# Performance work log

Measured on AMD Instinct MI355X. Metric: run time of the kernel, lower is better.

The kernel has to match this reference:

```python
import jax, jax.numpy as jnp
import numpy as np

B, D, H, C, V, SAMPLE_NUM = 4096, 1024, 512, 50, 4, 10000


def ds_combin_two(alpha1, alpha2, K):
    """Dempster-Shafer combination of two Dirichlet parameter sets [B, K]."""
    S1 = jnp.sum(alpha1, axis=1, keepdims=True)
    S2 = jnp.sum(alpha2, axis=1, keepdims=True)
    b1 = (alpha1 - 1.0) / S1
    b2 = (alpha2 - 1.0) / S2
    u1 = K / S1  # [B,1]
    u2 = K / S2
    # bb_sum - bb_diag computed without materializing [B,K,K] outer product:
    # sum_ij b1_i b2_j = sum(b1)*sum(b2); diag sum = sum_i b1_i b2_i
    Cconf = jnp.sum(b1, axis=1) * jnp.sum(b2, axis=1) - jnp.sum(b1 * b2, axis=1)  # [B]
    denom = (1.0 - Cconf)[:, None]
    b_a = (b1 * b2 + b1 * u2 + b2 * u1) / denom
    u_a = (u1 * u2) / denom  # [B,1]
    S_a = K / u_a
    e_a = b_a * S_a
    return e_a + 1.0


def setup_inputs() -> dict:
    key = jax.random.key(0)
    ks = jax.random.split(key, 8)
    x = jax.random.normal(ks[0], (V, B, D), dtype=jnp.float32)
    indexes = jax.random.randint(ks[1], (B,), 0, SAMPLE_NUM)
    W1 = jax.random.normal(ks[2], (V, D, H), dtype=jnp.float32) * (1.0 / np.sqrt(D))
    b1 = jax.random.normal(ks[3], (V, H), dtype=jnp.float32) * 0.01
    W2 = jax.random.normal(ks[4], (V, H, C), dtype=jnp.float32) * (1.0 / np.sqrt(H))
    b2 = jax.random.normal(ks[5], (V, C), dtype=jnp.float32) * 0.01
    # original init: identity per (view, sample); add small noise so the
    eye = jnp.eye(C, dtype=jnp.float32)
    matrixes = eye[None, None] + 0.01 * jax.random.normal(ks[6], (V, SAMPLE_NUM, C, C), dtype=jnp.float32)
    return {"x": x, "indexes": indexes, "W1": W1, "b1": b1, "W2": W2, "b2": b2, "matrixes": matrixes}


def reference(x, indexes, W1, b1, W2, b2, matrixes):
    K = W2.shape[-1]
    n_views = x.shape[0]
    # per-view classifier MLP: Linear->ReLU->Linear->Softplus
    h = jax.nn.relu(jnp.einsum("vbd,vdh->vbh", x, W1) + b1[:, None, :])
    evidence = jax.nn.softplus(jnp.einsum("vbh,vhc->vbc", h, W2) + b2[:, None, :])  # [V,B,C]
    # transferByMatrix (training path): per-sample gathered [C,C] matmul
    sel = matrixes[:, indexes]  # [V,B,C,C]
    transferred = jnp.einsum("vbc,vbcd->vbd", evidence, sel)  # [V,B,C]
    t_alpha = transferred + 1.0
    # sequential DS combination over views
    alpha_a = t_alpha[0]
    for v in range(1, n_views):
        alpha_a = ds_combin_two(alpha_a, t_alpha[v], K)
    evidence_a = alpha_a - 1.0  # [B,C]
    return transferred, evidence_a, evidence
```

## Files before the change

kernel.cpp:

```cpp
#include <hip/hip_runtime.h>
#include <hip/hip_bf16.h>
#include <math.h>

typedef unsigned short u16;
typedef __attribute__((ext_vector_type(8))) short bf16x8;
typedef __attribute__((ext_vector_type(4))) float f32x4;

#define DEVI __device__ __forceinline__

constexpr int NV = 4;
constexpr int NB = 4096;
constexpr int ND = 1024;
constexpr int NH = 512;
constexpr int NC = 50;
constexpr int NSAMP = 10000;
constexpr int NCP = 64;

DEVI u16 to_bf16(float f) {
  union { float f; unsigned u; } v; v.f = f;
  unsigned r = v.u + 0x7fffu + ((v.u >> 16) & 1u);
  return (u16)(r >> 16);
}

DEVI u16 cvt_bf16(float f) {
  __hip_bfloat16 h = __float2bfloat16(f);
  return *reinterpret_cast<u16*>(&h);
}

DEVI float wsum(float x) {
#pragma unroll
  for (int m = 32; m > 0; m >>= 1) x += __shfl_xor(x, m, 64);
  return x;
}

#define GLD_LDS16(gsrc, ldst)                                                  \
  __builtin_amdgcn_global_load_lds(                                            \
      (const __attribute__((address_space(1))) void*)(gsrc),                   \
      (__attribute__((address_space(3))) void*)(ldst), 16, 0, 0)

__global__ __launch_bounds__(256) void k_prep(const float* __restrict__ W1,
                                              const float* __restrict__ W2,
                                              u16* __restrict__ W1T,
                                              u16* __restrict__ W2T) {
  __shared__ float tile[32][33];
  const int v = blockIdx.z;
  const int tx = threadIdx.x, ty = threadIdx.y;
  if (blockIdx.y < NH / 32) {
    const int d0 = blockIdx.x * 32;
    const int h0 = blockIdx.y * 32;
    const float* src = W1 + (size_t)v * ND * NH;
    u16* dst = W1T + (size_t)v * NH * ND;
#pragma unroll
    for (int j = 0; j < 32; j += 8)
      tile[ty + j][tx] = src[(size_t)(d0 + ty + j) * NH + h0 + tx];
    __syncthreads();
#pragma unroll
    for (int j = 0; j < 32; j += 8)
      dst[(size_t)(h0 + ty + j) * ND + d0 + tx] = to_bf16(tile[tx][ty + j]);
  } else {
    const int tid = ty * 32 + tx;
#pragma unroll
    for (int i = 0; i < 4; ++i) {
      int e = blockIdx.x * 1024 + i * 256 + tid;
      int h = e % NH;
      int c = e / NH;
      float val = (c < NC) ? W2[((size_t)v * NH + h) * NC + c] : 0.f;
      W2T[(size_t)v * NCP * NH + e] = to_bf16(val);
    }
  }
}

__global__ __launch_bounds__(512) void k_gemm1(const float* __restrict__ Xf,
                                               const u16* __restrict__ W1T,
                                               const float* __restrict__ b1,
                                               u16* __restrict__ Hb) {
  constexpr int BM = 128, BN = 256, BK = 32;
  const int v = blockIdx.z;
  const int m0 = blockIdx.x * BM;
  const int n0 = blockIdx.y * BN;
  __shared__ u16 As[BM][BK];
  __shared__ u16 Bs[BN][BK];
  const float* Ag = Xf + (size_t)v * NB * ND + (size_t)m0 * ND;
  const u16* Bg = W1T + (size_t)v * NH * ND + (size_t)n0 * ND;
  const int tid = threadIdx.x;
  const int lane = tid & 63;
  const int wv = tid >> 6;
  const int wr = wv >> 2, wc = wv & 3;
  const int rA = tid >> 2;
  const int cA = (tid & 3) * 8;

  f32x4 acc[4][4] = {};

  float4 pa0 = *(const float4*)(Ag + (size_t)rA * ND + cA);
  float4 pa1 = *(const float4*)(Ag + (size_t)rA * ND + cA + 4);

  for (int k0 = 0; k0 < ND; k0 += BK) {
    __syncthreads();
    {
      ushort4 u0, u1;
      u0.x = cvt_bf16(pa0.x); u0.y = cvt_bf16(pa0.y);
      u0.z = cvt_bf16(pa0.z); u0.w = cvt_bf16(pa0.w);
      u1.x = cvt_bf16(pa1.x); u1.y = cvt_bf16(pa1.y);
      u1.z = cvt_bf16(pa1.z); u1.w = cvt_bf16(pa1.w);
      *(ushort4*)&As[rA][cA]     = u0;
      *(ushort4*)&As[rA][cA + 4] = u1;
    }
#pragma unroll
    for (int i = 0; i < 2; ++i) {
      int s = tid + i * 512;
      GLD_LDS16(Bg + (size_t)(s >> 2) * ND + k0 + (s & 3) * 8,
                &Bs[s >> 2][(s & 3) * 8]);
    }
    __syncthreads();

    if (k0 + BK < ND) {
      pa0 = *(const float4*)(Ag + (size_t)rA * ND + k0 + BK + cA);
      pa1 = *(const float4*)(Ag + (size_t)rA * ND + k0 + BK + cA + 4);
    }

    const int fr = lane & 15;
    const int kb = (lane >> 4) * 8;
    bf16x8 af[4], bf[4];
#pragma unroll
    for (int mi = 0; mi < 4; ++mi)
      af[mi] = *(const bf16x8*)&As[wr * 64 + mi * 16 + fr][kb];
#pragma unroll
    for (int ni = 0; ni < 4; ++ni)
      bf[ni] = *(const bf16x8*)&Bs[wc * 64 + ni * 16 + fr][kb];
#pragma unroll
    for (int mi = 0; mi < 4; ++mi)
#pragma unroll
      for (int ni = 0; ni < 4; ++ni)
        acc[mi][ni] = __builtin_amdgcn_mfma_f32_16x16x32_bf16(
            af[mi], bf[ni], acc[mi][ni], 0, 0, 0);
  }

  const int frow = (lane >> 4) * 4;
  const int fcol = lane & 15;
#pragma unroll
  for (int mi = 0; mi < 4; ++mi) {
#pragma unroll
    for (int ni = 0; ni < 4; ++ni) {
      const int n = n0 + wc * 64 + ni * 16 + fcol;
      const float bias = b1[v * NH + n];
#pragma unroll
      for (int j = 0; j < 4; ++j) {
        const int m = m0 + wr * 64 + mi * 16 + frow + j;
        float val = fmaxf(acc[mi][ni][j] + bias, 0.f);
        Hb[(size_t)v * NB * NH + (size_t)m * NH + n] = to_bf16(val);
      }
    }
  }
}

__global__ __launch_bounds__(256) void k_gemm2(const u16* __restrict__ Hb,
                                               const u16* __restrict__ W2T,
                                               const float* __restrict__ b2,
                                               float* __restrict__ out_ev) {
  constexpr int BM = 64, BK = 32;
  const int v = blockIdx.z;
  const int m0 = blockIdx.x * BM;
  __shared__ u16 As[BM][BK];
  __shared__ u16 Bs[NCP][BK];
  const u16* Ag = Hb + (size_t)v * NB * NH + (size_t)m0 * NH;
  const u16* Bg = W2T + (size_t)v * NCP * NH;
  const int tid = threadIdx.x;
  const int lane = tid & 63;
  const int wv = tid >> 6;
  const int r = tid >> 2;
  const int c8 = (tid & 3) * 8;

  f32x4 acc[4] = {};

  for (int k0 = 0; k0 < NH; k0 += BK) {
    __syncthreads();
    GLD_LDS16(Ag + (size_t)r * NH + k0 + c8, &As[r][c8]);
    GLD_LDS16(Bg + (size_t)r * NH + k0 + c8, &Bs[r][c8]);
    __syncthreads();

    const int fr = lane & 15;
    const int kb = (lane >> 4) * 8;
    bf16x8 af = *(const bf16x8*)&As[wv * 16 + fr][kb];
#pragma unroll
    for (int ni = 0; ni < 4; ++ni) {
      bf16x8 bf = *(const bf16x8*)&Bs[ni * 16 + fr][kb];
      acc[ni] = __builtin_amdgcn_mfma_f32_16x16x32_bf16(af, bf, acc[ni], 0, 0, 0);
    }
  }

  const int frow = (lane >> 4) * 4;
  const int fcol = lane & 15;
#pragma unroll
  for (int ni = 0; ni < 4; ++ni) {
    const int n = ni * 16 + fcol;
    if (n < NC) {
      const float bias = b2[v * NC + n];
#pragma unroll
      for (int j = 0; j < 4; ++j) {
        const int m = m0 + wv * 16 + frow + j;
        float x = acc[ni][j] + bias;
        float sp = fmaxf(x, 0.f) + log1pf(expf(-fabsf(x)));
        out_ev[(size_t)v * NB * NC + (size_t)m * NC + n] = sp;
      }
    }
  }
}

__global__ __launch_bounds__(256) void k_tc(const float* __restrict__ evf,
                                            const float* __restrict__ mats,
                                            const int* __restrict__ idx,
                                            float* __restrict__ out_tr,
                                            float* __restrict__ out_ea) {
  const int b = blockIdx.x * 4 + (threadIdx.x >> 6);
  const int lane = threadIdx.x & 63;
  if (b >= NB) return;
  const bool act = lane < NC;
  const float Kf = (float)NC;
  const int ix = idx[b];

  float ta[NV];
#pragma unroll
  for (int v = 0; v < NV; ++v) {
    float acc = 0.f;
    if (act) {
      const float* e = evf + ((size_t)v * NB + b) * NC;
      const float* M = mats + ((size_t)v * NSAMP + ix) * NC * NC;
#pragma unroll
      for (int c = 0; c < NC; ++c)
        acc = fmaf(e[c], M[c * NC + lane], acc);
      out_tr[((size_t)v * NB + b) * NC + lane] = acc;
    }
    ta[v] = act ? acc + 1.0f : 0.0f;
  }

  float alpha = ta[0];
#pragma unroll
  for (int v = 1; v < NV; ++v) {
    float a2 = ta[v];
    float S1 = wsum(act ? alpha : 0.f);
    float S2 = wsum(act ? a2 : 0.f);
    float b1v = act ? (alpha - 1.f) / S1 : 0.f;
    float b2v = act ? (a2 - 1.f) / S2 : 0.f;
    float u1 = Kf / S1, u2 = Kf / S2;
    float sb1 = wsum(b1v);
    float sb2 = wsum(b2v);
    float sb12 = wsum(b1v * b2v);
    float Cconf = sb1 * sb2 - sb12;
    float denom = 1.f - Cconf;
    float b_a = (b1v * b2v + b1v * u2 + b2v * u1) / denom;
    float u_a = u1 * u2 / denom;
    float S_a = Kf / u_a;
    alpha = b_a * S_a + 1.f;
  }
  if (act) out_ea[(size_t)b * NC + lane] = alpha - 1.f;
}

extern "C" void kernel_launch(void* const* d_in, const int* in_sizes, int n_in,
                              void* d_out, int out_size, void* d_ws, size_t ws_size,
                              hipStream_t stream) {
  const float *x = nullptr, *W1 = nullptr, *b1 = nullptr, *W2 = nullptr,
              *b2 = nullptr, *mats = nullptr;
  const int* idx = nullptr;
  for (int i = 0; i < n_in; ++i) {
    switch (in_sizes[i]) {
      case 16777216:  x    = (const float*)d_in[i]; break;
      case 4096:      idx  = (const int*)d_in[i];   break;
      case 2097152:   W1   = (const float*)d_in[i]; break;
      case 2048:      b1   = (const float*)d_in[i]; break;
      case 102400:    W2   = (const float*)d_in[i]; break;
      case 200:       b2   = (const float*)d_in[i]; break;
      case 100000000: mats = (const float*)d_in[i]; break;
      default: break;
    }
  }
  if (!x || !idx || !W1 || !b1 || !W2 || !b2 || !mats) return;

  char* ws = (char*)d_ws;
  u16* w1t = (u16*)(ws + 0);
  u16* w2t = (u16*)(ws + 4194304);
  u16* hb  = (u16*)(ws + 4456448);

  float* out_tr = (float*)d_out;
  float* out_ea = out_tr + (size_t)NV * NB * NC;
  float* out_ev = out_ea + (size_t)NB * NC;

  k_prep<<<dim3(32, NH / 32 + 1, NV), dim3(32, 8), 0, stream>>>(W1, W2, w1t, w2t);
  k_gemm1<<<dim3(NB / 128, NH / 256, NV), 512, 0, stream>>>(x, w1t, b1, hb);
  k_gemm2<<<dim3(NB / 64, 1, NV), 256, 0, stream>>>(hb, w2t, b2, out_ev);
  k_tc<<<NB / 4, 256, 0, stream>>>(out_ev, mats, idx, out_tr, out_ea);
}
```

Baseline: 89.41 us.

## Double-buffer LDS tiles in first GEMM with manual waitcnt pipelining

Converts the first GEMM's main loop to a double-buffered LDS pipeline. The next tile of A and B is staged into the alternate buffer while the current one is computed, using explicit s_waitcnt, s_barrier and sched_barrier to control overlap. The aim is to hide global-load and LDS-store latency behind the MFMA work and to drop one barrier per iteration. This doubles LDS use and depends on hand-counted vmcnt/lgkmcnt values, which makes a race possible if the counts are wrong.

```diff
diff --git a/kernel.cpp b/kernel.cpp
--- a/kernel.cpp
+++ b/kernel.cpp
@@ -75,11 +75,12 @@
                                                const float* __restrict__ b1,
                                                u16* __restrict__ Hb) {
   constexpr int BM = 128, BN = 256, BK = 32;
+  constexpr int NT = ND / BK;
   const int v = blockIdx.z;
   const int m0 = blockIdx.x * BM;
   const int n0 = blockIdx.y * BN;
-  __shared__ u16 As[BM][BK];
-  __shared__ u16 Bs[BN][BK];
+  __shared__ u16 As[2][BM][BK];
+  __shared__ u16 Bs[2][BN][BK];
   const float* Ag = Xf + (size_t)v * NB * ND + (size_t)m0 * ND;
   const u16* Bg = W1T + (size_t)v * NH * ND + (size_t)n0 * ND;
   const int tid = threadIdx.x;
@@ -90,50 +91,78 @@
   const int cA = (tid & 3) * 8;
 
   f32x4 acc[4][4] = {};
-
-  float4 pa0 = *(const float4*)(Ag + (size_t)rA * ND + cA);
-  float4 pa1 = *(const float4*)(Ag + (size_t)rA * ND + cA + 4);
-
-  for (int k0 = 0; k0 < ND; k0 += BK) {
-    __syncthreads();
-    {
-      ushort4 u0, u1;
-      u0.x = cvt_bf16(pa0.x); u0.y = cvt_bf16(pa0.y);
-      u0.z = cvt_bf16(pa0.z); u0.w = cvt_bf16(pa0.w);
-      u1.x = cvt_bf16(pa1.x); u1.y = cvt_bf16(pa1.y);
-      u1.z = cvt_bf16(pa1.z); u1.w = cvt_bf16(pa1.w);
-      *(ushort4*)&As[rA][cA]     = u0;
-      *(ushort4*)&As[rA][cA + 4] = u1;
-    }
+  float4 pa0, pa1;
+
+  auto LOAD_PA = [&](int k) {
+    pa0 = *(const float4*)(Ag + (size_t)rA * ND + k + cA);
+    pa1 = *(const float4*)(Ag + (size_t)rA * ND + k + cA + 4);
+  };
+  auto STAGE_A = [&](int buf) {
+    ushort4 u0, u1;
+    u0.x = cvt_bf16(pa0.x); u0.y = cvt_bf16(pa0.y);
+    u0.z = cvt_bf16(pa0.z); u0.w = cvt_bf16(pa0.w);
+    u1.x = cvt_bf16(pa1.x); u1.y = cvt_bf16(pa1.y);
+    u1.z = cvt_bf16(pa1.z); u1.w = cvt_bf16(pa1.w);
+    *(ushort4*)&As[buf][rA][cA]     = u0;
+    *(ushort4*)&As[buf][rA][cA + 4] = u1;
+  };
+  auto STAGE_B = [&](int buf, int k0) {
 #pragma unroll
     for (int i = 0; i < 2; ++i) {
       int s = tid + i * 512;
       GLD_LDS16(Bg + (size_t)(s >> 2) * ND + k0 + (s & 3) * 8,
-                &Bs[s >> 2][(s & 3) * 8]);
-    }
-    __syncthreads();
-
-    if (k0 + BK < ND) {
-      pa0 = *(const float4*)(Ag + (size_t)rA * ND + k0 + BK + cA);
-      pa1 = *(const float4*)(Ag + (size_t)rA * ND + k0 + BK + cA + 4);
-    }
-
+                &Bs[buf][s >> 2][(s & 3) * 8]);
+    }
+  };
+  auto COMPUTE = [&](int buf) {
     const int fr = lane & 15;
     const int kb = (lane >> 4) * 8;
     bf16x8 af[4], bf[4];
 #pragma unroll
     for (int mi = 0; mi < 4; ++mi)
-      af[mi] = *(const bf16x8*)&As[wr * 64 + mi * 16 + fr][kb];
+      af[mi] = *(const bf16x8*)&As[buf][wr * 64 + mi * 16 + fr][kb];
 #pragma unroll
     for (int ni = 0; ni < 4; ++ni)
-      bf[ni] = *(const bf16x8*)&Bs[wc * 64 + ni * 16 + fr][kb];
+      bf[ni] = *(const bf16x8*)&Bs[buf][wc * 64 + ni * 16 + fr][kb];
 #pragma unroll
     for (int mi = 0; mi < 4; ++mi)
 #pragma unroll
       for (int ni = 0; ni < 4; ++ni)
         acc[mi][ni] = __builtin_amdgcn_mfma_f32_16x16x32_bf16(
             af[mi], bf[ni], acc[mi][ni], 0, 0, 0);
-  }
+  };
+
+  LOAD_PA(0);
+  STAGE_B(0, 0);
+  STAGE_A(0);
+  LOAD_PA(BK);
+
+  for (int t = 0; t < NT - 2; ++t) {
+    const int cur = t & 1, nxt = cur ^ 1;
+    __builtin_amdgcn_s_barrier();
+    STAGE_A(nxt);
+    LOAD_PA((t + 2) * BK);
+    STAGE_B(nxt, (t + 1) * BK);
+    asm volatile("s_waitcnt vmcnt(4) lgkmcnt(2)" ::: "memory");
+    __builtin_amdgcn_sched_barrier(0);
+    __builtin_amdgcn_s_barrier();
+    __builtin_amdgcn_sched_barrier(0);
+    COMPUTE(cur);
+  }
+  __builtin_amdgcn_s_barrier();
+  STAGE_A(1);
+  STAGE_B(1, (NT - 1) * BK);
+  asm volatile("s_waitcnt vmcnt(2) lgkmcnt(2)" ::: "memory");
+  __builtin_amdgcn_sched_barrier(0);
+  __builtin_amdgcn_s_barrier();
+  __builtin_amdgcn_sched_barrier(0);
+  COMPUTE(0);
+  __builtin_amdgcn_s_barrier();
+  asm volatile("s_waitcnt vmcnt(0) lgkmcnt(0)" ::: "memory");
+  __builtin_amdgcn_sched_barrier(0);
+  __builtin_amdgcn_s_barrier();
+  __builtin_amdgcn_sched_barrier(0);
+  COMPUTE(1);
 
   const int frow = (lane >> 4) * 4;
   const int fcol = lane & 15;
```

After: 92.70 us. 3.7% more time.
